# Optimization experiments

Measured on AMD Instinct MI355X. Metric: run time of the kernel, lower is better.

## Reference

```python
import jax, jax.numpy as jnp
import numpy as np

B, T, U, D, V = 8, 200, 50, 512, 1024

def setup_inputs() -> dict:
    key = jax.random.key(0)
    k1, k2, k3, k4 = jax.random.split(key, 4)
    encoder_out = jax.random.normal(k1, (B, T, D), dtype=jnp.float32)
    predictor_out = jax.random.normal(k2, (B, U, D), dtype=jnp.float32)
    # nn.Linear(D, V): weight [V, D], bias [V]
    W = jax.random.normal(k3, (V, D), dtype=jnp.float32) / np.sqrt(D)
    b = jax.random.normal(k4, (V,), dtype=jnp.float32) * 0.01
    return {"encoder_out": encoder_out, "predictor_out": predictor_out, "W": W, "b": b}

def reference(encoder_out, predictor_out, W, b):
    # out[b,t,u,:] = Linear(enc[b,t,:] + pred[b,u,:])
    joint = encoder_out[:, :, None, :] + predictor_out[:, None, :, :]  # [B,T,U,D]
    return jnp.einsum('btud,vd->btuv', joint, W) + b  # [B,T,U,V]
```

## Files before the change

kernel.cpp:

```cpp
#include <hip/hip_runtime.h>
#include <hip/hip_bf16.h>


typedef __attribute__((ext_vector_type(8))) short bf16x8;
typedef __attribute__((ext_vector_type(4))) float f32x4;

__device__ __forceinline__ unsigned short f2bf(float f) {
    union { float f; unsigned int u; } x; x.f = f;
    unsigned int u = x.u;
    unsigned int r = (u + 0x7fffu + ((u >> 16) & 1u)) >> 16;
    return (unsigned short)r;
}

__global__ __launch_bounds__(256) void cvt_kernel(const float* __restrict__ enc,
                                                  const float* __restrict__ pred,
                                                  const float* __restrict__ W,
                                                  unsigned short* __restrict__ dst) {
    int i4 = (blockIdx.x * 256 + threadIdx.x) * 4;
    const float* src;
    if (i4 < 819200)        src = enc  + i4;
    else if (i4 < 1024000)  src = pred + (i4 - 819200);
    else                    src = W    + (i4 - 1024000);
    float4 f = *(const float4*)src;
    ushort4 o;
    o.x = f2bf(f.x); o.y = f2bf(f.y); o.z = f2bf(f.z); o.w = f2bf(f.w);
    *(ushort4*)(dst + i4) = o;
}

__global__ __launch_bounds__(256) void gemm_kernel(const unsigned short* __restrict__ A,
                                                   const unsigned short* __restrict__ Wb,
                                                   float* __restrict__ EP) {
    int lane = threadIdx.x & 63;
    int wave = threadIdx.x >> 6;
    int quad = lane >> 4;
    int l16  = lane & 15;
    int mw = blockIdx.x * 64 + wave * 16;
    int n0 = blockIdx.y * 64;
    int row = mw + l16; if (row > 1999) row = 1999;
    const bf16x8* ap = (const bf16x8*)(A  + row * 512 + quad * 8);
    const bf16x8* b0 = (const bf16x8*)(Wb + (n0      + l16) * 512 + quad * 8);
    const bf16x8* b1 = (const bf16x8*)(Wb + (n0 + 16 + l16) * 512 + quad * 8);
    const bf16x8* b2 = (const bf16x8*)(Wb + (n0 + 32 + l16) * 512 + quad * 8);
    const bf16x8* b3 = (const bf16x8*)(Wb + (n0 + 48 + l16) * 512 + quad * 8);
    f32x4 acc0 = {0.f,0.f,0.f,0.f}, acc1 = {0.f,0.f,0.f,0.f};
    f32x4 acc2 = {0.f,0.f,0.f,0.f}, acc3 = {0.f,0.f,0.f,0.f};
#pragma unroll
    for (int kk = 0; kk < 16; ++kk) {
        bf16x8 a = ap[kk * 4];
        acc0 = __builtin_amdgcn_mfma_f32_16x16x32_bf16(a, b0[kk * 4], acc0, 0, 0, 0);
        acc1 = __builtin_amdgcn_mfma_f32_16x16x32_bf16(a, b1[kk * 4], acc1, 0, 0, 0);
        acc2 = __builtin_amdgcn_mfma_f32_16x16x32_bf16(a, b2[kk * 4], acc2, 0, 0, 0);
        acc3 = __builtin_amdgcn_mfma_f32_16x16x32_bf16(a, b3[kk * 4], acc3, 0, 0, 0);
    }
#pragma unroll
    for (int i = 0; i < 4; ++i) {
        int r = mw + quad * 4 + i;
        if (r < 2000) {
            float* er = EP + r * 1024 + l16;
            er[n0     ] = acc0[i];
            er[n0 + 16] = acc1[i];
            er[n0 + 32] = acc2[i];
            er[n0 + 48] = acc3[i];
        }
    }
}

__global__ __launch_bounds__(512) void bcast_kernel(const float* __restrict__ EP,
                                                    const float* __restrict__ bias,
                                                    float* __restrict__ out) {
    int bt   = blockIdx.x;
    int b    = bt / 200;
    int half = threadIdx.x >> 8;
    int v0   = (threadIdx.x & 255) * 4;

    f32x4 e = *(const f32x4*)(EP + bt * 1024 + v0);
    e += *(const f32x4*)(bias + v0);

    const float* Pb = EP + (size_t)(1600 + b * 50 + half) * 1024 + v0;
    float*       ob = out + (size_t)bt * 51200 + (size_t)half * 1024 + v0;

    f32x4 p = *(const f32x4*)Pb;
#pragma unroll
    for (int i = 0; i < 24; ++i) {
        f32x4 pn = *(const f32x4*)(Pb + (i + 1) * 2048);
        *(f32x4*)(ob + i * 2048) = e + p;
        p = pn;
    }
    *(f32x4*)(ob + 24 * 2048) = e + p;
}

__global__ __launch_bounds__(256) void fallback_kernel(const float* __restrict__ enc,
                                                       const float* __restrict__ pred,
                                                       const float* __restrict__ W,
                                                       const float* __restrict__ bias,
                                                       float* __restrict__ out) {
    int btu = blockIdx.x;
    int u  = btu % 50;
    int bt = btu / 50;
    int b  = bt / 200;
    __shared__ float j[512];
    const float* e = enc  + bt * 512;
    const float* p = pred + (b * 50 + u) * 512;
    for (int k = threadIdx.x; k < 512; k += 256) j[k] = e[k] + p[k];
    __syncthreads();
    int v = threadIdx.x * 4;
    float a0 = bias[v], a1 = bias[v + 1], a2 = bias[v + 2], a3 = bias[v + 3];
    for (int k = 0; k < 512; k += 4) {
        float4 jk = *(const float4*)(j + k);
        float4 w0 = *(const float4*)(W + (v + 0) * 512 + k);
        float4 w1 = *(const float4*)(W + (v + 1) * 512 + k);
        float4 w2 = *(const float4*)(W + (v + 2) * 512 + k);
        float4 w3 = *(const float4*)(W + (v + 3) * 512 + k);
        a0 += jk.x * w0.x + jk.y * w0.y + jk.z * w0.z + jk.w * w0.w;
        a1 += jk.x * w1.x + jk.y * w1.y + jk.z * w1.z + jk.w * w1.w;
        a2 += jk.x * w2.x + jk.y * w2.y + jk.z * w2.z + jk.w * w2.w;
        a3 += jk.x * w3.x + jk.y * w3.y + jk.z * w3.z + jk.w * w3.w;
    }
    size_t o = (size_t)btu * 1024 + v;
    out[o] = a0; out[o + 1] = a1; out[o + 2] = a2; out[o + 3] = a3;
}

extern "C" void kernel_launch(void* const* d_in, const int* in_sizes, int n_in,
                              void* d_out, int out_size, void* d_ws, size_t ws_size,
                              hipStream_t stream) {
    const float* enc  = (const float*)d_in[0];
    const float* pred = (const float*)d_in[1];
    const float* W    = (const float*)d_in[2];
    const float* bias = (const float*)d_in[3];
    float* out = (float*)d_out;

    const size_t NEED = 2048000u + 1048576u + 8192000u;
    if (ws_size >= NEED) {
        unsigned short* AB = (unsigned short*)d_ws;
        float* EP = (float*)((char*)d_ws + 2048000 + 1048576);
        cvt_kernel<<<1512, 256, 0, stream>>>(enc, pred, W, AB);
        gemm_kernel<<<dim3(32, 16), 256, 0, stream>>>(AB, AB + 1024000, EP);
        bcast_kernel<<<1600, 512, 0, stream>>>(EP, bias, out);
    } else {
        fallback_kernel<<<80000, 256, 0, stream>>>(enc, pred, W, bias, out);
    }
}
```

Measured before the change: 357.8 us.

## Fuse encoder projection GEMM into broadcast kernel, keep separate predictor GEMM

The GEMM kernel now projects only the 400 predictor rows. The encoder-row projection is computed inside a new fused kernel, which stages the 16x128 result tile in LDS, adds bias and writes the broadcast output directly. This drops the EP write and re-read for encoder rows and one kernel's worth of separate work. In exchange the output-writing grid changes shape: 800 blocks of 256 threads, each writing 32 rows of 50 u-strided stores, where before there were 1600 blocks of 512 threads.

```diff
diff --git a/kernel.cpp b/kernel.cpp
--- a/kernel.cpp
+++ b/kernel.cpp
@@ -29,12 +29,13 @@
 
 __global__ __launch_bounds__(256) void gemm_kernel(const unsigned short* __restrict__ A,
                                                    const unsigned short* __restrict__ Wb,
-                                                   float* __restrict__ EP) {
+                                                   float* __restrict__ EP,
+                                                   int row_base) {
     int lane = threadIdx.x & 63;
     int wave = threadIdx.x >> 6;
     int quad = lane >> 4;
     int l16  = lane & 15;
-    int mw = blockIdx.x * 64 + wave * 16;
+    int mw = row_base + blockIdx.x * 64 + wave * 16;
     int n0 = blockIdx.y * 64;
     int row = mw + l16; if (row > 1999) row = 1999;
     const bf16x8* ap = (const bf16x8*)(A  + row * 512 + quad * 8);
@@ -65,28 +66,60 @@
     }
 }
 
-__global__ __launch_bounds__(512) void bcast_kernel(const float* __restrict__ EP,
+__global__ __launch_bounds__(256) void fused_kernel(const unsigned short* __restrict__ AB,
+                                                    const unsigned short* __restrict__ Wb,
+                                                    const float* __restrict__ EP,
                                                     const float* __restrict__ bias,
                                                     float* __restrict__ out) {
-    int bt   = blockIdx.x;
-    int b    = bt / 200;
-    int half = threadIdx.x >> 8;
-    int v0   = (threadIdx.x & 255) * 4;
+    __shared__ f32x4 e_lds4[16][32];
+    int lane = threadIdx.x & 63;
+    int wave = threadIdx.x >> 6;
+    int quad = lane >> 4;
+    int l16  = lane & 15;
+    int bt0 = blockIdx.x * 16;
+    int v0  = blockIdx.y * 128;
 
-    f32x4 e = *(const f32x4*)(EP + bt * 1024 + v0);
-    e += *(const f32x4*)(bias + v0);
+    int nb = v0 + wave * 32;
+    const bf16x8* ap  = (const bf16x8*)(AB + (bt0 + l16) * 512 + quad * 8);
+    const bf16x8* bp0 = (const bf16x8*)(Wb + (nb      + l16) * 512 + quad * 8);
+    const bf16x8* bp1 = (const bf16x8*)(Wb + (nb + 16 + l16) * 512 + quad * 8);
+    f32x4 acc0 = {0.f,0.f,0.f,0.f}, acc1 = {0.f,0.f,0.f,0.f};
+#pragma unroll
+    for (int kk = 0; kk < 16; ++kk) {
+        bf16x8 a = ap[kk * 4];
+        acc0 = __builtin_amdgcn_mfma_f32_16x16x32_bf16(a, bp0[kk * 4], acc0, 0, 0, 0);
+        acc1 = __builtin_amdgcn_mfma_f32_16x16x32_bf16(a, bp1[kk * 4], acc1, 0, 0, 0);
+    }
 
-    const float* Pb = EP + (size_t)(1600 + b * 50 + half) * 1024 + v0;
-    float*       ob = out + (size_t)bt * 51200 + (size_t)half * 1024 + v0;
+    float* ef = (float*)&e_lds4[0][0];
+    int cl0 = wave * 32 + l16;
+#pragma unroll
+    for (int i = 0; i < 4; ++i) {
+        int rl = quad * 4 + i;
+        ef[rl * 128 + cl0     ] = acc0[i];
+        ef[rl * 128 + cl0 + 16] = acc1[i];
+    }
+    __syncthreads();
 
-    f32x4 p = *(const f32x4*)Pb;
-#pragma unroll
-    for (int i = 0; i < 24; ++i) {
-        f32x4 pn = *(const f32x4*)(Pb + (i + 1) * 2048);
-        *(f32x4*)(ob + i * 2048) = e + p;
-        p = pn;
+    int half = lane >> 5;
+    int l32  = lane & 31;
+    f32x4 bv = *(const f32x4*)(bias + v0 + l32 * 4);
+    int r0 = wave * 4 + half;
+    int r1 = r0 + 2;
+    f32x4 e0 = e_lds4[r0][l32] + bv;
+    f32x4 e1 = e_lds4[r1][l32] + bv;
+    int btA = bt0 + r0, btB = bt0 + r1;
+    const float* P0 = EP + (size_t)(1600 + (btA / 200) * 50) * 1024 + v0 + l32 * 4;
+    const float* P1 = EP + (size_t)(1600 + (btB / 200) * 50) * 1024 + v0 + l32 * 4;
+    float* o0 = out + (size_t)btA * 51200 + v0 + l32 * 4;
+    float* o1 = out + (size_t)btB * 51200 + v0 + l32 * 4;
+#pragma unroll 5
+    for (int u = 0; u < 50; ++u) {
+        f32x4 p0 = *(const f32x4*)(P0 + u * 1024);
+        f32x4 p1 = *(const f32x4*)(P1 + u * 1024);
+        *(f32x4*)(o0 + u * 1024) = e0 + p0;
+        *(f32x4*)(o1 + u * 1024) = e1 + p1;
     }
-    *(f32x4*)(ob + 24 * 2048) = e + p;
 }
 
 __global__ __launch_bounds__(256) void fallback_kernel(const float* __restrict__ enc,
@@ -134,8 +167,8 @@
         unsigned short* AB = (unsigned short*)d_ws;
         float* EP = (float*)((char*)d_ws + 2048000 + 1048576);
         cvt_kernel<<<1512, 256, 0, stream>>>(enc, pred, W, AB);
-        gemm_kernel<<<dim3(32, 16), 256, 0, stream>>>(AB, AB + 1024000, EP);
-        bcast_kernel<<<1600, 512, 0, stream>>>(EP, bias, out);
+        gemm_kernel<<<dim3(7, 16), 256, 0, stream>>>(AB, AB + 1024000, EP, 1600);
+        fused_kernel<<<dim3(100, 8), 256, 0, stream>>>(AB, AB + 1024000, EP, bias, out);
     } else {
         fallback_kernel<<<80000, 256, 0, stream>>>(enc, pred, W, bias, out);
     }
```

New measurement: 367.6 us. +2.7%, slower.
